# Optimization experiments

Hardware: AMD Instinct MI355X
Metric: run time of the kernel (lower is better)

Reference implementation:

```python
import math
import jax, jax.numpy as jnp
import numpy as np

B, LQ, LK, D = 32, 2048, 2048, 128

def setup_inputs() -> dict:
    key = jax.random.key(0)
    kq, kk, kv, kl = jax.random.split(key, 4)
    queries = jax.random.normal(kq, (B, LQ, D), dtype=jnp.float32)
    keys = jax.random.normal(kk, (B, LK, D), dtype=jnp.float32)
    values = jax.random.normal(kv, (B, LK, D), dtype=jnp.float32)
    # per-batch valid lengths in [1, LK] (min 1 so every row has a valid key)
    valid_lens = jax.random.randint(kl, (B,), 1, LK + 1, dtype=jnp.int32)
    return {"queries": queries, "keys": keys, "values": values, "valid_lens": valid_lens}

def reference(queries, keys, values, valid_lens):
    d = keys.shape[-1]
    # [B, LQ, LK] scaled scores
    scores = jnp.einsum("bqd,bkd->bqk", queries, keys) / math.sqrt(d)
    # valid_lens is 1D per-batch -> broadcast over query positions (torch repeat(shape[1]))
    mask = jnp.arange(scores.shape[-1])[None, None, :] < valid_lens[:, None, None]
    scores = jnp.where(mask, scores, -jnp.inf)
    attn = jax.nn.softmax(scores, axis=-1)
    # dropout p=0.0 -> identity
    return jnp.einsum("bqk,bkv->bqv", attn, values)
```

## Files before the change

kernel.cpp:

```cpp
#include <hip/hip_runtime.h>
#include <hip/hip_bf16.h>
#include <math.h>


#define BATCH 32
#define SEQL  2048
#define DIM   128
#define KVB   64
#define QTILE 128
#define KBUF  16384
#define VBUF  16384
#define EPSTR 34

typedef __attribute__((ext_vector_type(8)))  __bf16 bf8;
typedef __attribute__((ext_vector_type(16))) float  f16v;
typedef __attribute__((ext_vector_type(2)))  unsigned int u32x2;
typedef unsigned int u32;

static __device__ __forceinline__ f16v mfma32(bf8 a, bf8 b, f16v c) {
  return __builtin_amdgcn_mfma_f32_32x32x16_bf16(a, b, c, 0, 0, 0);
}
static __device__ __forceinline__ u32 cvtpk(float lo, float hi) {
  u32 r; asm("v_cvt_pk_bf16_f32 %0, %1, %2" : "=v"(r) : "v"(lo), "v"(hi)); return r;
}
static __device__ __forceinline__ void plswap(u32& a, u32& b) {
#if __has_builtin(__builtin_amdgcn_permlane32_swap)
  auto r = __builtin_amdgcn_permlane32_swap(a, b, false, false);
  a = (u32)r[0]; b = (u32)r[1];
#else
  asm("s_nop 1\n\tv_permlane32_swap_b32 %0, %1" : "+v"(a), "+v"(b));
#endif
}
static __device__ __forceinline__ float xmax(float x) {
  u32 a = __builtin_bit_cast(u32, x), c = a;
  plswap(a, c);
  return fmaxf(__builtin_bit_cast(float, a), __builtin_bit_cast(float, c));
}
static __device__ __forceinline__ float xadd(float x) {
  u32 a = __builtin_bit_cast(u32, x), c = a;
  plswap(a, c);
  return __builtin_bit_cast(float, a) + __builtin_bit_cast(float, c);
}
static __device__ __forceinline__ float fexp2(float x) {
#if __has_builtin(__builtin_amdgcn_exp2f)
  return __builtin_amdgcn_exp2f(x);
#else
  return exp2f(x);
#endif
}
static __device__ __forceinline__ u32 ext16(u32x2 v, int c) {
  u32 w = ((c >> 1) & 1) ? v[1] : v[0];
  return (c & 1) ? (w >> 16) : (w & 0xffffu);
}

#define MKPB(ARR, BASE, DST) {                                   \
    u32 x0 = cvtpk(ARR[BASE+0], ARR[BASE+1]);                    \
    u32 y0 = cvtpk(ARR[BASE+4], ARR[BASE+5]);                    \
    plswap(x0, y0);                                              \
    u32 x1 = cvtpk(ARR[BASE+2], ARR[BASE+3]);                    \
    u32 y1 = cvtpk(ARR[BASE+6], ARR[BASE+7]);                    \
    plswap(x1, y1);                                              \
    union { u32 u[4]; bf8 v; } uu;                               \
    uu.u[0] = x0; uu.u[1] = x1; uu.u[2] = y0; uu.u[3] = y1;      \
    DST = uu.v; }

__global__ __launch_bounds__(256, 2)
void attn_fwd(const float* __restrict__ Q, const float* __restrict__ K,
              const float* __restrict__ V, const int* __restrict__ vlen,
              float* __restrict__ O)
{
  __shared__ __align__(128) char smem[2*KBUF + 2*VBUF];

  const int tid  = threadIdx.x;
  const int w    = tid >> 6;
  const int lane = tid & 63;
  const int ql   = lane & 31;
  const int hi   = lane >> 5;
  const int tw   = tid >> 5;
  const int d4   = tid & 31;

  const int fid  = blockIdx.x;
  const int bb   = (fid & 7) * 4 + ((fid >> 3) >> 4);
  const int q0   = ((fid >> 3) & 15) * QTILE;

  const int valid = vlen[bb];
  const int nt    = (valid + KVB - 1) / KVB;

  const float QS = 0.08838834764831845f * 1.4426950408889634f;

  bf8 qf[8];
  {
    const float* qp = Q + ((size_t)bb * SEQL + q0 + w*32 + ql) * DIM + hi*8;
    #pragma unroll
    for (int kb = 0; kb < 8; ++kb) {
      float4 a = *(const float4*)(qp + kb*16);
      float4 c = *(const float4*)(qp + kb*16 + 4);
      union { u32 u[4]; bf8 v; } t;
      t.u[0] = cvtpk(a.x*QS, a.y*QS);
      t.u[1] = cvtpk(a.z*QS, a.w*QS);
      t.u[2] = cvtpk(c.x*QS, c.y*QS);
      t.u[3] = cvtpk(c.z*QS, c.w*QS);
      qf[kb] = t.v;
    }
  }

  f16v acc[4] = {};
  float m = -INFINITY, l = 0.f;

  u32x2 kreg[8], vA[4], vB[4];
  const float* Kb = K + ((size_t)bb * SEQL) * DIM;
  const float* Vb = V + ((size_t)bb * SEQL) * DIM;

  auto LOAD = [&](int t) {
    const int kv0 = t * KVB;
    #pragma unroll
    for (int i = 0; i < 8; ++i) {
      float4 x = *(const float4*)(Kb + (size_t)(kv0 + i*8 + tw) * DIM + d4*4);
      kreg[i][0] = cvtpk(x.x, x.y); kreg[i][1] = cvtpk(x.z, x.w);
    }
    #pragma unroll
    for (int i = 0; i < 4; ++i) {
      const int kvA = kv0 + 16*i + 2*tw;
      float4 x = *(const float4*)(Vb + (size_t)kvA * DIM + d4*4);
      float4 y = *(const float4*)(Vb + (size_t)(kvA + 1) * DIM + d4*4);
      vA[i][0] = cvtpk(x.x, x.y); vA[i][1] = cvtpk(x.z, x.w);
      vB[i][0] = cvtpk(y.x, y.y); vB[i][1] = cvtpk(y.z, y.w);
    }
  };

  const int kwb = tw*256 + ((d4*8) ^ (tw << 4));
  auto STORE = [&](int s) {
    char* kb_ = smem + s*KBUF;
    char* vb_ = smem + 2*KBUF + s*VBUF;
    #pragma unroll
    for (int i = 0; i < 8; ++i)
      *(u32x2*)(kb_ + i*2048 + kwb) = kreg[i];
    #pragma unroll
    for (int i = 0; i < 4; ++i) {
      const int p = 8*i + tw;
      #pragma unroll
      for (int j = 0; j < 4; ++j) {
        const int c   = (j + (d4 >> 2)) & 3;
        const int row = 4*d4 + c;
        u32 val = ext16(vA[i], c) | (ext16(vB[i], c) << 16);
        *(u32*)(vb_ + row*128 + ((4*p) ^ ((row & 7) << 4))) = val;
      }
    }
  };

  LOAD(0); STORE(0);
  __syncthreads();

  for (int t = 0; t < nt; ++t) {
    const int  sel  = t & 1;
    const bool more = (t + 1 < nt);
    if (more) LOAD(t + 1);

    const char* kb_ = smem + sel*KBUF;
    const char* vb_ = smem + 2*KBUF + sel*VBUF;

    f16v s0v = {}, s1v = {};
    {
      const int rb = ql * 256;
      #pragma unroll
      for (int kb = 0; kb < 8; ++kb) {
        const int off = rb + (((kb << 5) | (hi << 4)) ^ ((ql & 7) << 4));
        bf8 k0 = *(const bf8*)(kb_ + off);
        bf8 k1 = *(const bf8*)(kb_ + off + 8192);
        s0v = mfma32(k0, qf[kb], s0v);
        s1v = mfma32(k1, qf[kb], s1v);
      }
    }

    const int kv0 = t * KVB;
    if (kv0 + KVB > valid) {
      #pragma unroll
      for (int r = 0; r < 16; ++r) {
        const int kvl = (r & 3) + 8*(r >> 2) + 4*hi;
        if (kv0 + kvl >= valid)      s0v[r] = -INFINITY;
        if (kv0 + 32 + kvl >= valid) s1v[r] = -INFINITY;
      }
    }

    float c0 = fmaxf(s0v[0], s1v[0]);
    float c1 = fmaxf(s0v[1], s1v[1]);
    float c2 = fmaxf(s0v[2], s1v[2]);
    float c3 = fmaxf(s0v[3], s1v[3]);
    #pragma unroll
    for (int r = 4; r < 16; r += 4) {
      c0 = fmaxf(c0, fmaxf(s0v[r],     s1v[r]));
      c1 = fmaxf(c1, fmaxf(s0v[r + 1], s1v[r + 1]));
      c2 = fmaxf(c2, fmaxf(s0v[r + 2], s1v[r + 2]));
      c3 = fmaxf(c3, fmaxf(s0v[r + 3], s1v[r + 3]));
    }
    const float tmax = xmax(fmaxf(fmaxf(c0, c1), fmaxf(c2, c3)));

    if (!__all(tmax <= m + 8.0f)) {
      const float mn = fmaxf(m, tmax);
      const float al = fexp2(m - mn);
      #pragma unroll
      for (int d = 0; d < 4; ++d) acc[d] *= al;
      l *= al;
      m = mn;
    }

    float p0[16], p1[16];
    #pragma unroll
    for (int r = 0; r < 16; ++r) {
      p0[r] = fexp2(s0v[r] - m);
      p1[r] = fexp2(s1v[r] - m);
    }
    {
      float d0 = p0[0] + p1[0], d1 = p0[1] + p1[1];
      float d2 = p0[2] + p1[2], d3 = p0[3] + p1[3];
      #pragma unroll
      for (int r = 4; r < 16; r += 4) {
        d0 += p0[r]     + p1[r];
        d1 += p0[r + 1] + p1[r + 1];
        d2 += p0[r + 2] + p1[r + 2];
        d3 += p0[r + 3] + p1[r + 3];
      }
      l += xadd((d0 + d1) + (d2 + d3));
    }

    bf8 pb[4];
    MKPB(p0, 0, pb[0]); MKPB(p0, 8, pb[1]);
    MKPB(p1, 0, pb[2]); MKPB(p1, 8, pb[3]);

    #pragma unroll
    for (int db = 0; db < 4; ++db) {
      #pragma unroll
      for (int ks = 0; ks < 4; ++ks) {
        const int off = (db*32 + ql)*128 + (((ks << 5) | (hi << 4)) ^ ((ql & 7) << 4));
        bf8 vf = *(const bf8*)(vb_ + off);
        acc[db] = mfma32(vf, pb[ks], acc[db]);
      }
    }

    if (more) STORE(sel ^ 1);
    __syncthreads();
  }

  const float invl = 1.0f / l;
  float* ep = (float*)smem + (size_t)w * (32 * EPSTR);
  const size_t orow0 = (size_t)bb * SEQL + q0 + w*32;
  #pragma unroll
  for (int db = 0; db < 4; ++db) {
    #pragma unroll
    for (int r = 0; r < 16; ++r) {
      const int dloc = (r & 3) + 8*(r >> 2) + 4*hi;
      ep[ql*EPSTR + dloc] = acc[db][r] * invl;
    }
    #pragma unroll
    for (int pq = 0; pq < 4; ++pq) {
      const int qr = (lane >> 3) + pq*8;
      const float* rp = ep + qr*EPSTR + (lane & 7)*4;
      float2 x0 = *(const float2*)rp;
      float2 x1 = *(const float2*)(rp + 2);
      float4 st = make_float4(x0.x, x0.y, x1.x, x1.y);
      *(float4*)(O + (orow0 + qr)*DIM + db*32 + (lane & 7)*4) = st;
    }
  }
}

extern "C" void kernel_launch(void* const* d_in, const int* in_sizes, int n_in,
                              void* d_out, int out_size, void* d_ws, size_t ws_size,
                              hipStream_t stream) {
  const float* Q  = (const float*)d_in[0];
  const float* K  = (const float*)d_in[1];
  const float* V  = (const float*)d_in[2];
  const int*   vl = (const int*)d_in[3];
  float* O = (float*)d_out;
  attn_fwd<<<dim3(512), dim3(256), 0, stream>>>(Q, K, V, vl, O);
}
```

Measured before the change: 219.9 us.

## Split KV loop across two warp groups per block and merge softmax partials

```diff
diff --git a/kernel.cpp b/kernel.cpp
--- a/kernel.cpp
+++ b/kernel.cpp
@@ -9,7 +9,8 @@
 #define KVB   64
 #define QTILE 128
 #define KBUF  16384
-#define VBUF  16384
+#define GBUF  32768
+#define MLOFF 65536
 #define EPSTR 34
 
 typedef __attribute__((ext_vector_type(8)))  __bf16 bf8;
@@ -64,19 +65,21 @@
     uu.u[0] = x0; uu.u[1] = x1; uu.u[2] = y0; uu.u[3] = y1;      \
     DST = uu.v; }
 
-__global__ __launch_bounds__(256, 2)
+__global__ __launch_bounds__(512, 4)
 void attn_fwd(const float* __restrict__ Q, const float* __restrict__ K,
               const float* __restrict__ V, const int* __restrict__ vlen,
               float* __restrict__ O)
 {
-  __shared__ __align__(128) char smem[2*KBUF + 2*VBUF];
+  __shared__ __align__(128) char smem[MLOFF + 1024];
 
   const int tid  = threadIdx.x;
   const int w    = tid >> 6;
+  const int gidx = w >> 2;
+  const int wl   = w & 3;
   const int lane = tid & 63;
   const int ql   = lane & 31;
   const int hi   = lane >> 5;
-  const int tw   = tid >> 5;
+  const int twg  = (tid >> 5) & 7;
   const int d4   = tid & 31;
 
   const int fid  = blockIdx.x;
@@ -85,12 +88,13 @@
 
   const int valid = vlen[bb];
   const int nt    = (valid + KVB - 1) / KVB;
+  const int S     = (nt + 1) >> 1;
 
   const float QS = 0.08838834764831845f * 1.4426950408889634f;
 
   bf8 qf[8];
   {
-    const float* qp = Q + ((size_t)bb * SEQL + q0 + w*32 + ql) * DIM + hi*8;
+    const float* qp = Q + ((size_t)bb * SEQL + q0 + wl*32 + ql) * DIM + hi*8;
     #pragma unroll
     for (int kb = 0; kb < 8; ++kb) {
       float4 a = *(const float4*)(qp + kb*16);
@@ -111,16 +115,19 @@
   const float* Kb = K + ((size_t)bb * SEQL) * DIM;
   const float* Vb = V + ((size_t)bb * SEQL) * DIM;
 
+  char* const kbuf = smem + gidx * GBUF;
+  char* const vbuf = kbuf + KBUF;
+
   auto LOAD = [&](int t) {
     const int kv0 = t * KVB;
     #pragma unroll
     for (int i = 0; i < 8; ++i) {
-      float4 x = *(const float4*)(Kb + (size_t)(kv0 + i*8 + tw) * DIM + d4*4);
+      float4 x = *(const float4*)(Kb + (size_t)(kv0 + i*8 + twg) * DIM + d4*4);
       kreg[i][0] = cvtpk(x.x, x.y); kreg[i][1] = cvtpk(x.z, x.w);
     }
     #pragma unroll
     for (int i = 0; i < 4; ++i) {
-      const int kvA = kv0 + 16*i + 2*tw;
+      const int kvA = kv0 + 16*i + 2*twg;
       float4 x = *(const float4*)(Vb + (size_t)kvA * DIM + d4*4);
       float4 y = *(const float4*)(Vb + (size_t)(kvA + 1) * DIM + d4*4);
       vA[i][0] = cvtpk(x.x, x.y); vA[i][1] = cvtpk(x.z, x.w);
@@ -128,137 +135,171 @@
     }
   };
 
-  const int kwb = tw*256 + ((d4*8) ^ (tw << 4));
-  auto STORE = [&](int s) {
-    char* kb_ = smem + s*KBUF;
-    char* vb_ = smem + 2*KBUF + s*VBUF;
+  const int kwb = twg*256 + ((d4*8) ^ (twg << 4));
+  auto STORE = [&]() {
     #pragma unroll
     for (int i = 0; i < 8; ++i)
-      *(u32x2*)(kb_ + i*2048 + kwb) = kreg[i];
+      *(u32x2*)(kbuf + i*2048 + kwb) = kreg[i];
     #pragma unroll
     for (int i = 0; i < 4; ++i) {
-      const int p = 8*i + tw;
+      const int p = 8*i + twg;
       #pragma unroll
       for (int j = 0; j < 4; ++j) {
         const int c   = (j + (d4 >> 2)) & 3;
         const int row = 4*d4 + c;
         u32 val = ext16(vA[i], c) | (ext16(vB[i], c) << 16);
-        *(u32*)(vb_ + row*128 + ((4*p) ^ ((row & 7) << 4))) = val;
+        *(u32*)(vbuf + row*128 + ((4*p) ^ ((row & 7) << 4))) = val;
       }
     }
   };
 
-  LOAD(0); STORE(0);
+  if (gidx < nt) { LOAD(gidx); STORE(); }
   __syncthreads();
 
-  for (int t = 0; t < nt; ++t) {
-    const int  sel  = t & 1;
-    const bool more = (t + 1 < nt);
-    if (more) LOAD(t + 1);
-
-    const char* kb_ = smem + sel*KBUF;
-    const char* vb_ = smem + 2*KBUF + sel*VBUF;
-
-    f16v s0v = {}, s1v = {};
-    {
-      const int rb = ql * 256;
-      #pragma unroll
-      for (int kb = 0; kb < 8; ++kb) {
-        const int off = rb + (((kb << 5) | (hi << 4)) ^ ((ql & 7) << 4));
-        bf8 k0 = *(const bf8*)(kb_ + off);
-        bf8 k1 = *(const bf8*)(kb_ + off + 8192);
-        s0v = mfma32(k0, qf[kb], s0v);
-        s1v = mfma32(k1, qf[kb], s1v);
-      }
-    }
-
-    const int kv0 = t * KVB;
-    if (kv0 + KVB > valid) {
+  for (int s = 0; s < S; ++s) {
+    const int  t   = gidx + 2*s;
+    const bool act = t < nt;
+    const bool nxt = t + 2 < nt;
+
+    if (act) {
+      if (nxt) LOAD(t + 2);
+
+      f16v s0v = {}, s1v = {};
+      {
+        const int rb = ql * 256;
+        #pragma unroll
+        for (int kb = 0; kb < 8; ++kb) {
+          const int off = rb + (((kb << 5) | (hi << 4)) ^ ((ql & 7) << 4));
+          bf8 k0 = *(const bf8*)(kbuf + off);
+          bf8 k1 = *(const bf8*)(kbuf + off + 8192);
+          s0v = mfma32(k0, qf[kb], s0v);
+          s1v = mfma32(k1, qf[kb], s1v);
+        }
+      }
+
+      const int kv0 = t * KVB;
+      if (kv0 + KVB > valid) {
+        #pragma unroll
+        for (int r = 0; r < 16; ++r) {
+          const int kvl = (r & 3) + 8*(r >> 2) + 4*hi;
+          if (kv0 + kvl >= valid)      s0v[r] = -INFINITY;
+          if (kv0 + 32 + kvl >= valid) s1v[r] = -INFINITY;
+        }
+      }
+
+      float c0 = fmaxf(s0v[0], s1v[0]);
+      float c1 = fmaxf(s0v[1], s1v[1]);
+      float c2 = fmaxf(s0v[2], s1v[2]);
+      float c3 = fmaxf(s0v[3], s1v[3]);
+      #pragma unroll
+      for (int r = 4; r < 16; r += 4) {
+        c0 = fmaxf(c0, fmaxf(s0v[r],     s1v[r]));
+        c1 = fmaxf(c1, fmaxf(s0v[r + 1], s1v[r + 1]));
+        c2 = fmaxf(c2, fmaxf(s0v[r + 2], s1v[r + 2]));
+        c3 = fmaxf(c3, fmaxf(s0v[r + 3], s1v[r + 3]));
+      }
+      const float tmax = xmax(fmaxf(fmaxf(c0, c1), fmaxf(c2, c3)));
+
+      if (!__all(tmax <= m + 8.0f)) {
+        const float mn = fmaxf(m, tmax);
+        const float al = fexp2(m - mn);
+        #pragma unroll
+        for (int d = 0; d < 4; ++d) acc[d] *= al;
+        l *= al;
+        m = mn;
+      }
+
+      float p0[16], p1[16];
       #pragma unroll
       for (int r = 0; r < 16; ++r) {
-        const int kvl = (r & 3) + 8*(r >> 2) + 4*hi;
-        if (kv0 + kvl >= valid)      s0v[r] = -INFINITY;
-        if (kv0 + 32 + kvl >= valid) s1v[r] = -INFINITY;
-      }
-    }
-
-    float c0 = fmaxf(s0v[0], s1v[0]);
-    float c1 = fmaxf(s0v[1], s1v[1]);
-    float c2 = fmaxf(s0v[2], s1v[2]);
-    float c3 = fmaxf(s0v[3], s1v[3]);
-    #pragma unroll
-    for (int r = 4; r < 16; r += 4) {
-      c0 = fmaxf(c0, fmaxf(s0v[r],     s1v[r]));
-      c1 = fmaxf(c1, fmaxf(s0v[r + 1], s1v[r + 1]));
-      c2 = fmaxf(c2, fmaxf(s0v[r + 2], s1v[r + 2]));
-      c3 = fmaxf(c3, fmaxf(s0v[r + 3], s1v[r + 3]));
-    }
-    const float tmax = xmax(fmaxf(fmaxf(c0, c1), fmaxf(c2, c3)));
-
-    if (!__all(tmax <= m + 8.0f)) {
-      const float mn = fmaxf(m, tmax);
-      const float al = fexp2(m - mn);
-      #pragma unroll
-      for (int d = 0; d < 4; ++d) acc[d] *= al;
-      l *= al;
-      m = mn;
-    }
-
-    float p0[16], p1[16];
-    #pragma unroll
-    for (int r = 0; r < 16; ++r) {
-      p0[r] = fexp2(s0v[r] - m);
-      p1[r] = fexp2(s1v[r] - m);
-    }
-    {
-      float d0 = p0[0] + p1[0], d1 = p0[1] + p1[1];
-      float d2 = p0[2] + p1[2], d3 = p0[3] + p1[3];
-      #pragma unroll
-      for (int r = 4; r < 16; r += 4) {
-        d0 += p0[r]     + p1[r];
-        d1 += p0[r + 1] + p1[r + 1];
-        d2 += p0[r + 2] + p1[r + 2];
-        d3 += p0[r + 3] + p1[r + 3];
-      }
-      l += xadd((d0 + d1) + (d2 + d3));
-    }
-
-    bf8 pb[4];
-    MKPB(p0, 0, pb[0]); MKPB(p0, 8, pb[1]);
-    MKPB(p1, 0, pb[2]); MKPB(p1, 8, pb[3]);
-
+        p0[r] = fexp2(s0v[r] - m);
+        p1[r] = fexp2(s1v[r] - m);
+      }
+      {
+        float d0 = p0[0] + p1[0], d1 = p0[1] + p1[1];
+        float d2 = p0[2] + p1[2], d3 = p0[3] + p1[3];
+        #pragma unroll
+        for (int r = 4; r < 16; r += 4) {
+          d0 += p0[r]     + p1[r];
+          d1 += p0[r + 1] + p1[r + 1];
+          d2 += p0[r + 2] + p1[r + 2];
+          d3 += p0[r + 3] + p1[r + 3];
+        }
+        l += xadd((d0 + d1) + (d2 + d3));
+      }
+
+      bf8 pb[4];
+      MKPB(p0, 0, pb[0]); MKPB(p0, 8, pb[1]);
+      MKPB(p1, 0, pb[2]); MKPB(p1, 8, pb[3]);
+
+      #pragma unroll
+      for (int db = 0; db < 4; ++db) {
+        #pragma unroll
+        for (int ks = 0; ks < 4; ++ks) {
+          const int off = (db*32 + ql)*128 + (((ks << 5) | (hi << 4)) ^ ((ql & 7) << 4));
+          bf8 vf = *(const bf8*)(vbuf + off);
+          acc[db] = mfma32(vf, pb[ks], acc[db]);
+        }
+      }
+    }
+
+    __syncthreads();
+    if (nxt) STORE();
+    __syncthreads();
+  }
+
+  if (gidx == 1) {
+    float* pr = (float*)(smem + wl * KBUF);
     #pragma unroll
     for (int db = 0; db < 4; ++db) {
       #pragma unroll
-      for (int ks = 0; ks < 4; ++ks) {
-        const int off = (db*32 + ql)*128 + (((ks << 5) | (hi << 4)) ^ ((ql & 7) << 4));
-        bf8 vf = *(const bf8*)(vb_ + off);
-        acc[db] = mfma32(vf, pb[ks], acc[db]);
-      }
-    }
-
-    if (more) STORE(sel ^ 1);
-    __syncthreads();
-  }
-
-  const float invl = 1.0f / l;
-  float* ep = (float*)smem + (size_t)w * (32 * EPSTR);
-  const size_t orow0 = (size_t)bb * SEQL + q0 + w*32;
-  #pragma unroll
-  for (int db = 0; db < 4; ++db) {
-    #pragma unroll
-    for (int r = 0; r < 16; ++r) {
-      const int dloc = (r & 3) + 8*(r >> 2) + 4*hi;
-      ep[ql*EPSTR + dloc] = acc[db][r] * invl;
-    }
-    #pragma unroll
-    for (int pq = 0; pq < 4; ++pq) {
-      const int qr = (lane >> 3) + pq*8;
-      const float* rp = ep + qr*EPSTR + (lane & 7)*4;
-      float2 x0 = *(const float2*)rp;
-      float2 x1 = *(const float2*)(rp + 2);
-      float4 st = make_float4(x0.x, x0.y, x1.x, x1.y);
-      *(float4*)(O + (orow0 + qr)*DIM + db*32 + (lane & 7)*4) = st;
+      for (int r = 0; r < 16; ++r) {
+        const int dloc = (r & 3) + 8*(r >> 2) + 4*hi;
+        pr[(db*32 + dloc)*32 + ql] = acc[db][r];
+      }
+    }
+    if (hi == 0)
+      ((float2*)(smem + MLOFF))[wl*32 + ql] = make_float2(m, l);
+  }
+  __syncthreads();
+  if (gidx == 0) {
+    const float2 ml2 = ((const float2*)(smem + MLOFF))[wl*32 + ql];
+    const float mf = fmaxf(m, ml2.x);
+    const float w1 = fexp2(m - mf);
+    const float w2 = fexp2(ml2.x - mf);
+    const float* pr = (const float*)(smem + wl * KBUF);
+    #pragma unroll
+    for (int db = 0; db < 4; ++db) {
+      #pragma unroll
+      for (int r = 0; r < 16; ++r) {
+        const int dloc = (r & 3) + 8*(r >> 2) + 4*hi;
+        acc[db][r] = acc[db][r]*w1 + pr[(db*32 + dloc)*32 + ql]*w2;
+      }
+    }
+    l = l*w1 + ml2.y*w2;
+  }
+  __syncthreads();
+
+  if (gidx == 0) {
+    const float invl = 1.0f / l;
+    float* ep = (float*)smem + (size_t)wl * (32 * EPSTR);
+    const size_t orow0 = (size_t)bb * SEQL + q0 + wl*32;
+    #pragma unroll
+    for (int db = 0; db < 4; ++db) {
+      #pragma unroll
+      for (int r = 0; r < 16; ++r) {
+        const int dloc = (r & 3) + 8*(r >> 2) + 4*hi;
+        ep[ql*EPSTR + dloc] = acc[db][r] * invl;
+      }
+      #pragma unroll
+      for (int pq = 0; pq < 4; ++pq) {
+        const int qr = (lane >> 3) + pq*8;
+        const float* rp = ep + qr*EPSTR + (lane & 7)*4;
+        float2 x0 = *(const float2*)rp;
+        float2 x1 = *(const float2*)(rp + 2);
+        float4 st = make_float4(x0.x, x0.y, x1.x, x1.y);
+        *(float4*)(O + (orow0 + qr)*DIM + db*32 + (lane & 7)*4) = st;
+      }
     }
   }
 }
@@ -271,5 +312,5 @@
   const float* V  = (const float*)d_in[2];
   const int*   vl = (const int*)d_in[3];
   float* O = (float*)d_out;
-  attn_fwd<<<dim3(512), dim3(256), 0, stream>>>(Q, K, V, vl, O);
-}
+  attn_fwd<<<dim3(512), dim3(512), 0, stream>>>(Q, K, V, vl, O);
+}
```

Measured after the change: 462.5 us. +110.4%, slower.
